# Optimization experiments

Measured on AMD Instinct MI355X. Metric: run time of the kernel, lower is better.

The kernel has to match this reference:

```python
import jax, jax.numpy as jnp
import numpy as np

R = 5                       # kernels_radius
D = 2 * R + 1               # kernels_diameter
KERNELS_DESC = [
    {"weight": 0.9, "xy": 6.0, "image": 0.1},
    {"weight": 0.1, "xy": 6.0},
]


def _unfold(t, r):
    """torch F.unfold with padding=r, stride=1 -> [N, C, D, D, H, W]."""
    N, C, H, W = t.shape
    d = 2 * r + 1
    tp = jnp.pad(t, ((0, 0), (0, 0), (r, r), (r, r)))
    # fixed small loop over D*D kernel offsets (121), not over data dims
    pats = jnp.stack(
        [tp[:, :, i:i + H, j:j + W] for i in range(d) for j in range(d)],
        axis=2,
    )
    return pats.reshape(N, C, d, d, H, W)


def reference(x, y_hat):
    N, _, H, W = x.shape
    dt = x.dtype
    # xy coordinate feature [N, 2, H, W]: (col index, row index)
    cols = jnp.broadcast_to(jnp.arange(W, dtype=dt)[None, :], (H, W))
    rows = jnp.broadcast_to(jnp.arange(H, dtype=dt)[:, None], (H, W))
    xy = jnp.broadcast_to(jnp.stack([cols, rows], 0)[None], (N, 2, H, W))

    kernels = jnp.zeros((N, 1, D, D, H, W), dtype=dt)
    for desc in KERNELS_DESC:
        feats = []
        for modality, sigma in desc.items():
            if modality == 'weight':
                continue
            f = xy if modality == 'xy' else x
            feats.append(f / sigma)
        features = jnp.concatenate(feats, axis=1)          # [N, c, H, W]
        k = _unfold(features, R)                           # [N, c, D, D, H, W]
        k = k - k[:, :, R, R][:, :, None, None]            # diff to window center
        k = jnp.exp((-0.5 * k ** 2).sum(axis=1, keepdims=True))
        k = k.at[:, :, R, R].set(0.0)                      # zero self-affinity
        kernels = kernels + desc['weight'] * k

    Cy = y_hat.shape[1]
    yu = _unfold(y_hat, R)                                  # [N, Cy, D, D, H, W]
    prod = (kernels * yu).reshape(N, Cy, D * D, H, W).sum(axis=2)
    loss = kernels.sum() - (prod * y_hat).sum()
    denom = jnp.asarray(N * H * W, dtype=dt)
    return loss / denom


def setup_inputs() -> dict:
    key = jax.random.key(0)
    k1, k2 = jax.random.split(key)
    x = jax.random.normal(k1, (4, 3, 128, 128), dtype=jnp.float32)
    y_hat = jax.random.uniform(k2, (4, 21, 128, 128), dtype=jnp.float32)
    return {"x": x, "y_hat": y_hat}
```

## Files before the change

kernel.cpp:

```cpp
#include <hip/hip_runtime.h>

constexpr int IMG_H = 128;
constexpr int IMG_W = 128;
constexpr int N_IMG = 4;
constexpr int CXCH = 3;
constexpr int CYCH = 21;
constexpr int RAD = 5;
constexpr int DIA = 11;
constexpr int TILE_H = 8;
constexpr int TILE_W = 16;
constexpr int PT_H = TILE_H + 2 * RAD;
constexpr int PT_W = TILE_W + 2 * RAD;
constexpr int NPIX = PT_H * PT_W;
constexpr int NPIXT = TILE_H * TILE_W;
constexpr int NGROUP = 4;
constexpr int NTHREADS = NPIXT * NGROUP;
constexpr int NPAIR = 60;
constexpr int PPG = NPAIR / NGROUP;
constexpr int HW = IMG_H * IMG_W;

__global__ __launch_bounds__(NTHREADS, 4)
void gcrf_kernel(const float* __restrict__ x, const float* __restrict__ y,
                 float* __restrict__ out) {
    __shared__ __align__(16) float sy[NPIX * 20];
    __shared__ __align__(16) float sx[NPIX * 4];
    __shared__ int   s_pk[NPAIR];
    __shared__ float s_e1[NPAIR];
    __shared__ float s_red[NTHREADS / 64];

    const int tid = threadIdx.x;
    const int n = blockIdx.z;
    const int h0 = blockIdx.y * TILE_H;
    const int w0 = blockIdx.x * TILE_W;

    const float* xb = x + (size_t)n * CXCH * HW;
    const float* yb = y + (size_t)n * CYCH * HW;

    if (tid < NPAIR) {
        int di, dj;
        if (tid < 5) { di = 0; dj = tid + 1; }
        else         { int m = tid - 5; di = 1 + m / 11; dj = m % 11 - 5; }
        s_pk[tid] = (di << 8) | (dj + 8);
        s_e1[tid] = __expf(-0.5f * (float)(di * di + dj * dj) * (1.0f / 36.0f));
    }

    for (int p = tid; p < NPIX; p += NTHREADS) {
        int ti = p / PT_W, tj = p - ti * PT_W;
        int gh = h0 + ti - RAD, gw = w0 + tj - RAD;
        bool inb = ((unsigned)gh < (unsigned)IMG_H) && ((unsigned)gw < (unsigned)IMG_W);
        int gofs = gh * IMG_W + gw;
        float v[CYCH];
        #pragma unroll
        for (int c = 0; c < CYCH; c++) v[c] = inb ? yb[c * HW + gofs] : 0.0f;
        float xv[CXCH];
        #pragma unroll
        for (int c = 0; c < CXCH; c++) xv[c] = inb ? xb[c * HW + gofs] : 0.0f;
        #pragma unroll
        for (int q = 0; q < 5; q++) {
            *(float4*)&sy[p * 20 + q * 4] =
                make_float4(v[q * 4 + 0], v[q * 4 + 1], v[q * 4 + 2], v[q * 4 + 3]);
        }
        *(float4*)&sx[p * 4] = make_float4(xv[0], xv[1], xv[2], v[20]);
    }
    __syncthreads();

    const int g = tid >> 7;
    const int pix = tid & (NPIXT - 1);
    const int tx = pix & (TILE_W - 1);
    const int ty = pix >> 4;
    const int h = h0 + ty, w = w0 + tx;
    const int cp = (ty + RAD) * PT_W + (tx + RAD);

    const float4 cx4 = *(const float4*)&sx[cp * 4];
    float yc[20];
    #pragma unroll
    for (int q = 0; q < 5; q++) {
        float4 t = *(const float4*)&sy[cp * 20 + q * 4];
        yc[q * 4 + 0] = t.x; yc[q * 4 + 1] = t.y;
        yc[q * 4 + 2] = t.z; yc[q * 4 + 3] = t.w;
    }

    float acc = 0.0f;
    if (g == 0) {
        int i0 = max(0, RAD - h), i1 = min(DIA - 1, IMG_H - 1 - h + RAD);
        int j0 = max(0, RAD - w), j1 = min(DIA - 1, IMG_W - 1 - w + RAD);
        int n_oob = DIA * DIA - (i1 - i0 + 1) * (j1 - j0 + 1);
        if (n_oob > 0) {
            float oxy = (float)(h * h + w * w) * (1.0f / 36.0f);
            float s2c = cx4.x * cx4.x + cx4.y * cx4.y + cx4.z * cx4.z;
            float kvo = __expf(-0.5f * oxy) * (0.9f * __expf(-50.0f * s2c) + 0.1f);
            acc = (float)n_oob * kvo;
        }
    }

    float accp = 0.0f;
    #pragma unroll
    for (int t = 0; t < PPG; t++) {
        int k = g * PPG + t;
        int pk = s_pk[k];
        float e1 = s_e1[k];
        int di = pk >> 8, dj = (pk & 255) - 8;
        int p = cp + di * PT_W + dj;
        float4 xq = *(const float4*)&sx[p * 4];
        float dot = xq.w * cx4.w;
        #pragma unroll
        for (int q = 0; q < 5; q++) {
            float4 tt = *(const float4*)&sy[p * 20 + q * 4];
            dot += tt.x * yc[q * 4 + 0] + tt.y * yc[q * 4 + 1] +
                   tt.z * yc[q * 4 + 2] + tt.w * yc[q * 4 + 3];
        }
        float d0 = xq.x - cx4.x, d1 = xq.y - cx4.y, d2 = xq.z - cx4.z;
        float s2 = d0 * d0 + d1 * d1 + d2 * d2;
        bool inb = ((h + di) < IMG_H) && ((unsigned)(w + dj) < (unsigned)IMG_W);
        float e = inb ? e1 : 0.0f;
        float kv = e * (0.9f * __expf(-50.0f * s2) + 0.1f);
        accp += kv * (1.0f - dot);
    }

    float total = acc + 2.0f * accp;

    #pragma unroll
    for (int s = 32; s > 0; s >>= 1) total += __shfl_down(total, s, 64);
    if ((tid & 63) == 0) s_red[tid >> 6] = total;
    __syncthreads();
    if (tid == 0) {
        float bs = 0.0f;
        #pragma unroll
        for (int wv = 0; wv < NTHREADS / 64; wv++) bs += s_red[wv];
        atomicAdd(out, bs * (1.0f / (float)(N_IMG * HW)));
    }
}

extern "C" void kernel_launch(void* const* d_in, const int* in_sizes, int n_in,
                              void* d_out, int out_size, void* d_ws, size_t ws_size,
                              hipStream_t stream) {
    const float* x = (const float*)d_in[0];
    const float* y = (const float*)d_in[1];
    float* out = (float*)d_out;
    hipMemsetAsync(out, 0, sizeof(float), stream);
    dim3 grid(IMG_W / TILE_W, IMG_H / TILE_H, N_IMG);
    gcrf_kernel<<<grid, NTHREADS, 0, stream>>>(x, y, out);
}
```

Measured before the change: 76.90 us.

## Store tile features as packed fp16 and use fdot2 for channel dot products

Shared-memory tiles for y and x are converted from fp32 to packed half2 words, 12 words per pixel instead of 24 floats. The inner pair loop then loads three uint4 per neighbour and computes the 21-channel dot with v_dot2 fp16 instructions, which halves LDS traffic and ALU work. Neighbour offsets and boundary-masked weights are precomputed into registers. Storing x in fp16 costs precision, and with the exp(-50*s2) term the kernel values and the final loss could drift noticeably.

Measured after the change: 78.17 us. About the same (+1.7%).

```diff
diff --git a/kernel.cpp b/kernel.cpp
--- a/kernel.cpp
+++ b/kernel.cpp
@@ -1,4 +1,6 @@
 #include <hip/hip_runtime.h>
+
+typedef _Float16 half2_t __attribute__((ext_vector_type(2)));
 
 constexpr int IMG_H = 128;
 constexpr int IMG_W = 128;
@@ -18,12 +20,29 @@
 constexpr int NPAIR = 60;
 constexpr int PPG = NPAIR / NGROUP;
 constexpr int HW = IMG_H * IMG_W;
+constexpr int SYW = 12;
+
+
+__device__ __forceinline__ unsigned pkh(float a, float b) {
+    half2_t h; h.x = (_Float16)a; h.y = (_Float16)b;
+    unsigned u; __builtin_memcpy(&u, &h, 4); return u;
+}
+__device__ __forceinline__ half2_t uph(unsigned u) {
+    half2_t h; __builtin_memcpy(&h, &u, 4); return h;
+}
+__device__ __forceinline__ float dot2(unsigned a, half2_t b, float c) {
+#if __has_builtin(__builtin_amdgcn_fdot2)
+    return __builtin_amdgcn_fdot2(uph(a), b, c, false);
+#else
+    half2_t ah = uph(a);
+    return c + (float)ah.x * (float)b.x + (float)ah.y * (float)b.y;
+#endif
+}
 
 __global__ __launch_bounds__(NTHREADS, 4)
 void gcrf_kernel(const float* __restrict__ x, const float* __restrict__ y,
                  float* __restrict__ out) {
-    __shared__ __align__(16) float sy[NPIX * 20];
-    __shared__ __align__(16) float sx[NPIX * 4];
+    __shared__ __align__(16) unsigned syh[NPIX * SYW];
     __shared__ int   s_pk[NPAIR];
     __shared__ float s_e1[NPAIR];
     __shared__ float s_red[NTHREADS / 64];
@@ -37,9 +56,8 @@
     const float* yb = y + (size_t)n * CYCH * HW;
 
     if (tid < NPAIR) {
-        int di, dj;
-        if (tid < 5) { di = 0; dj = tid + 1; }
-        else         { int m = tid - 5; di = 1 + m / 11; dj = m % 11 - 5; }
+        int di = tid < 5 ? 0 : 1 + (tid - 5) / 11;
+        int dj = tid < 5 ? tid + 1 : (tid - 5) % 11 - 5;
         s_pk[tid] = (di << 8) | (dj + 8);
         s_e1[tid] = __expf(-0.5f * (float)(di * di + dj * dj) * (1.0f / 36.0f));
     }
@@ -55,12 +73,15 @@
         float xv[CXCH];
         #pragma unroll
         for (int c = 0; c < CXCH; c++) xv[c] = inb ? xb[c * HW + gofs] : 0.0f;
+        unsigned d[SYW];
         #pragma unroll
-        for (int q = 0; q < 5; q++) {
-            *(float4*)&sy[p * 20 + q * 4] =
-                make_float4(v[q * 4 + 0], v[q * 4 + 1], v[q * 4 + 2], v[q * 4 + 3]);
-        }
-        *(float4*)&sx[p * 4] = make_float4(xv[0], xv[1], xv[2], v[20]);
+        for (int q = 0; q < 10; q++) d[q] = pkh(v[2 * q], v[2 * q + 1]);
+        d[10] = pkh(xv[0], xv[1]);
+        d[11] = pkh(xv[2], v[20]);
+        unsigned* dst = &syh[p * SYW];
+        *(uint4*)&dst[0] = make_uint4(d[0], d[1], d[2], d[3]);
+        *(uint4*)&dst[4] = make_uint4(d[4], d[5], d[6], d[7]);
+        *(uint4*)&dst[8] = make_uint4(d[8], d[9], d[10], d[11]);
     }
     __syncthreads();
 
@@ -70,15 +91,18 @@
     const int ty = pix >> 4;
     const int h = h0 + ty, w = w0 + tx;
     const int cp = (ty + RAD) * PT_W + (tx + RAD);
+    const unsigned* base = &syh[cp * SYW];
 
-    const float4 cx4 = *(const float4*)&sx[cp * 4];
-    float yc[20];
-    #pragma unroll
-    for (int q = 0; q < 5; q++) {
-        float4 t = *(const float4*)&sy[cp * 20 + q * 4];
-        yc[q * 4 + 0] = t.x; yc[q * 4 + 1] = t.y;
-        yc[q * 4 + 2] = t.z; yc[q * 4 + 3] = t.w;
-    }
+    uint4 c0 = *(const uint4*)&base[0];
+    uint4 c1 = *(const uint4*)&base[4];
+    uint4 c2 = *(const uint4*)&base[8];
+    half2_t yc[10];
+    yc[0] = uph(c0.x); yc[1] = uph(c0.y); yc[2] = uph(c0.z); yc[3] = uph(c0.w);
+    yc[4] = uph(c1.x); yc[5] = uph(c1.y); yc[6] = uph(c1.z); yc[7] = uph(c1.w);
+    yc[8] = uph(c2.x); yc[9] = uph(c2.y);
+    half2_t cxa = uph(c2.z), cxb = uph(c2.w);
+    const float cx0 = (float)cxa.x, cx1 = (float)cxa.y;
+    const float cx2 = (float)cxb.x, y20c = (float)cxb.y;
 
     float acc = 0.0f;
     if (g == 0) {
@@ -87,34 +111,42 @@
         int n_oob = DIA * DIA - (i1 - i0 + 1) * (j1 - j0 + 1);
         if (n_oob > 0) {
             float oxy = (float)(h * h + w * w) * (1.0f / 36.0f);
-            float s2c = cx4.x * cx4.x + cx4.y * cx4.y + cx4.z * cx4.z;
+            float s2c = cx0 * cx0 + cx1 * cx1 + cx2 * cx2;
             float kvo = __expf(-0.5f * oxy) * (0.9f * __expf(-50.0f * s2c) + 0.1f);
             acc = (float)n_oob * kvo;
         }
     }
 
-    float accp = 0.0f;
+    int offs[PPG]; float e1v[PPG];
     #pragma unroll
     for (int t = 0; t < PPG; t++) {
         int k = g * PPG + t;
         int pk = s_pk[k];
-        float e1 = s_e1[k];
         int di = pk >> 8, dj = (pk & 255) - 8;
-        int p = cp + di * PT_W + dj;
-        float4 xq = *(const float4*)&sx[p * 4];
-        float dot = xq.w * cx4.w;
-        #pragma unroll
-        for (int q = 0; q < 5; q++) {
-            float4 tt = *(const float4*)&sy[p * 20 + q * 4];
-            dot += tt.x * yc[q * 4 + 0] + tt.y * yc[q * 4 + 1] +
-                   tt.z * yc[q * 4 + 2] + tt.w * yc[q * 4 + 3];
-        }
-        float d0 = xq.x - cx4.x, d1 = xq.y - cx4.y, d2 = xq.z - cx4.z;
-        float s2 = d0 * d0 + d1 * d1 + d2 * d2;
-        bool inb = ((h + di) < IMG_H) && ((unsigned)(w + dj) < (unsigned)IMG_W);
-        float e = inb ? e1 : 0.0f;
-        float kv = e * (0.9f * __expf(-50.0f * s2) + 0.1f);
-        accp += kv * (1.0f - dot);
+        offs[t] = (di * PT_W + dj) * SYW;
+        bool inb = (h + di < IMG_H) & ((unsigned)(w + dj) < (unsigned)IMG_W);
+        e1v[t] = inb ? s_e1[k] : 0.0f;
+    }
+
+    float accp = 0.0f;
+    #pragma unroll
+    for (int t = 0; t < PPG; t++) {
+        const unsigned* q = base + offs[t];
+        uint4 a0 = *(const uint4*)&q[0];
+        uint4 a1 = *(const uint4*)&q[4];
+        uint4 a2 = *(const uint4*)&q[8];
+        float dot = 0.0f;
+        dot = dot2(a0.x, yc[0], dot); dot = dot2(a0.y, yc[1], dot);
+        dot = dot2(a0.z, yc[2], dot); dot = dot2(a0.w, yc[3], dot);
+        dot = dot2(a1.x, yc[4], dot); dot = dot2(a1.y, yc[5], dot);
+        dot = dot2(a1.z, yc[6], dot); dot = dot2(a1.w, yc[7], dot);
+        dot = dot2(a2.x, yc[8], dot); dot = dot2(a2.y, yc[9], dot);
+        half2_t xq = uph(a2.z), xr = uph(a2.w);
+        dot = fmaf((float)xr.y, y20c, dot);
+        float d0 = (float)xq.x - cx0, d1 = (float)xq.y - cx1, d2 = (float)xr.x - cx2;
+        float s2 = fmaf(d0, d0, fmaf(d1, d1, d2 * d2));
+        float kv = e1v[t] * fmaf(0.9f, __expf(-50.0f * s2), 0.1f);
+        accp = fmaf(kv, 1.0f - dot, accp);
     }
 
     float total = acc + 2.0f * accp;
```
